# Performance work log

Measured on AMD Instinct MI355X. Metric: run time of the kernel, lower is better.

## Reference

```python
import jax, jax.numpy as jnp
import numpy as np

C0, C1 = 16, 16              # multiplicities of 0e (scalar) and 1o (vector) irreps
FC_DIM = 32
N_EDGE_FEAT = 32
W_NUMEL = C0*C0 + C1*C0 + C0*C1 + C1*C1   # 1024 tensor-product path weights
D_IN = C0 + 3*C1             # 64


def split_irreps(x):
    # layout: [..., C0 scalars | C1 vectors flattened (C1,3)]
    s = x[..., :C0]
    v = x[..., C0:].reshape(x.shape[:-1] + (C1, 3))
    return s, v


def irrep_linear(s, v, ws, wv):
    # e3nn o3.Linear: per-irrep channel mixing, normalized by sqrt(fan_in)
    s2 = jnp.einsum('...i,io->...o', s, ws) / jnp.sqrt(jnp.float32(ws.shape[0]))
    v2 = jnp.einsum('...ix,io->...ox', v, wv) / jnp.sqrt(jnp.float32(wv.shape[0]))
    return s2, v2


def setup_inputs() -> dict:
    key = jax.random.key(0)
    ks = jax.random.split(key, 12)
    B, N = 2, 256
    node_attr = jax.random.normal(ks[0], (B, N, D_IN), jnp.float32)
    edge_attr = jax.random.normal(ks[1], (B, N, N, N_EDGE_FEAT), jnp.float32)
    edge_sh = jax.random.normal(ks[2], (B, N, N, 4), jnp.float32)  # 1x0e + 1x1o
    mask = jnp.ones((B, N), jnp.float32)
    # learned parameters
    w_lin_in_s = jax.random.normal(ks[3], (C0, C0), jnp.float32)
    w_lin_in_v = jax.random.normal(ks[4], (C1, C1), jnp.float32)
    fc_w1 = jax.random.normal(ks[5], (N_EDGE_FEAT, FC_DIM), jnp.float32) / np.sqrt(N_EDGE_FEAT)
    fc_b1 = jnp.zeros((FC_DIM,), jnp.float32)
    fc_w2 = jax.random.normal(ks[6], (FC_DIM, W_NUMEL), jnp.float32) / np.sqrt(FC_DIM)
    fc_b2 = jnp.zeros((W_NUMEL,), jnp.float32)
    w_lin_out_s = jax.random.normal(ks[7], (C0, C0), jnp.float32)
    w_lin_out_v = jax.random.normal(ks[8], (C1, C1), jnp.float32)
    return dict(node_attr=node_attr, edge_attr=edge_attr, edge_sh=edge_sh, mask=mask,
                w_lin_in_s=w_lin_in_s, w_lin_in_v=w_lin_in_v,
                fc_w1=fc_w1, fc_b1=fc_b1, fc_w2=fc_w2, fc_b2=fc_b2,
                w_lin_out_s=w_lin_out_s, w_lin_out_v=w_lin_out_v)


def tp_conv(node_attr, edge_attr, edge_sh, mask, w_lin_in_s, w_lin_in_v,
            fc_w1, fc_b1, fc_w2, fc_b2, w_lin_out_s, w_lin_out_v):
    B, N, _ = node_attr.shape
    s_na, v_na = split_irreps(node_attr)
    # lin_in
    s_in, v_in = irrep_linear(s_na, v_na, w_lin_in_s, w_lin_in_v)  # [B,N,C0], [B,N,C1,3]
    sh_s = edge_sh[..., 0]      # [B,N,N]
    sh_v = edge_sh[..., 1:4]    # [B,N,N,3]
    # edge MLP producing per-edge tensor-product path weights
    h = jax.nn.relu(edge_attr @ fc_w1 + fc_b1)
    w = h @ fc_w2 + fc_b2       # [B,N,N,W_NUMEL]
    off = 0
    w_ss = w[..., off:off+C0*C0].reshape(B, N, N, C0, C0); off += C0*C0
    w_vv = w[..., off:off+C1*C0].reshape(B, N, N, C1, C0); off += C1*C0
    w_sv = w[..., off:off+C0*C1].reshape(B, N, N, C0, C1); off += C0*C1
    w_vs = w[..., off:off+C1*C1].reshape(B, N, N, C1, C1)
    inv_fan = 1.0 / jnp.sqrt(jnp.float32(C0 + C1))
    # --- FullyConnectedTensorProduct (node i features x edge (i,j) SH) ---
    # 0e output: (0e x 0e -> 0e) + (1o x 1o -> 0e, CG = dot/sqrt(3))
    t_ss = jnp.einsum('bni,bnmio->bnmo', s_in, w_ss) * sh_s[..., None]
    dots = jnp.einsum('bnix,bnmx->bnmi', v_in, sh_v)
    t_vv = jnp.einsum('bnmi,bnmio->bnmo', dots, w_vv) / jnp.sqrt(3.0)
    tp_s = (t_ss + t_vv) * inv_fan                                  # [B,N,N,C0]
    # 1o output: (0e x 1o -> 1o) + (1o x 0e -> 1o)
    t_sv = jnp.einsum('bni,bnmio->bnmo', s_in, w_sv)[..., None] * sh_v[:, :, :, None, :]
    t_vs = jnp.einsum('bnix,bnmio->bnmox', v_in, w_vs) * sh_s[..., None, None]
    tp_v = (t_sv + t_vs) * inv_fan                                  # [B,N,N,C1,3]
    # --- masked reduction over source axis j (dim 2), excluding self ---
    m = mask[:, None, :] * (1.0 - jnp.eye(N, dtype=mask.dtype))[None]  # [B,N,N]
    dsum = jnp.sum(mask, axis=-1) - 1.0                                # [B]
    out_s = jnp.einsum('bnmo,bnm->bno', tp_s, m) / dsum[:, None, None]
    out_v = jnp.einsum('bnmox,bnm->bnox', tp_v, m) / dsum[:, None, None, None]
    # lin_out + residual (out dim == in dim, so F.pad is a no-op)
    out_s, out_v = irrep_linear(out_s, out_v, w_lin_out_s, w_lin_out_v)
    out_s = out_s + s_na
    out_v = out_v + v_na
    return jnp.concatenate([out_s, out_v.reshape(out_v.shape[0], out_v.shape[1], C1*3)], axis=-1)


def reference(node_attr, edge_attr, edge_sh, mask, w_lin_in_s, w_lin_in_v,
              fc_w1, fc_b1, fc_w2, fc_b2, w_lin_out_s, w_lin_out_v):
    return tp_conv(node_attr, edge_attr, edge_sh, mask, w_lin_in_s, w_lin_in_v,
                   fc_w1, fc_b1, fc_w2, fc_b2, w_lin_out_s, w_lin_out_v)
```

## Files before the change

kernel.cpp:

```cpp
#include <hip/hip_runtime.h>
#include <hip/hip_bf16.h>

typedef short short8 __attribute__((ext_vector_type(8)));
typedef float f32x4 __attribute__((ext_vector_type(4)));

__device__ __forceinline__ unsigned short f2bf(float f) {
    union { float f; unsigned int i; } v; v.f = f;
    unsigned int i = v.i;
    unsigned int r = (i + 0x7fffu + ((i >> 16) & 1u)) >> 16;
    return (unsigned short)r;
}

__global__ __launch_bounds__(256, 2)
void tpconv_kernel(const float* __restrict__ node_attr,
                   const float* __restrict__ edge_attr,
                   const float* __restrict__ edge_sh,
                   const float* __restrict__ mask,
                   const float* __restrict__ wlis,
                   const float* __restrict__ wliv,
                   const float* __restrict__ fc_w1,
                   const float* __restrict__ fc_b1,
                   const float* __restrict__ fc_w2,
                   const float* __restrict__ fc_b2,
                   const float* __restrict__ wlos,
                   const float* __restrict__ wlov,
                   float* __restrict__ out)
{
    const int node = blockIdx.x;
    const int b = node >> 8;
    const int n = node & 255;
    const int t = threadIdx.x;

    __shared__ __align__(16) unsigned short s_ea[256 * 32];
    __shared__ __align__(16) unsigned short s_w1t[32 * 32];
    __shared__ __align__(16) float s_wc[4 * 256];
    __shared__ float s_b1[32];
    __shared__ float s_wmask[4];
    __shared__ __align__(16) float s_wp[512];
    __shared__ float s_wp0[16];
    __shared__ __align__(16) float s_mom[128];
    __shared__ float s_mom0[4];
    __shared__ float s_scale;
    __shared__ float s_sin[16];
    __shared__ float s_vin[48];
    __shared__ __align__(16) float s_eff[8 * 256];
    __shared__ float s_pre[16];
    __shared__ float s_prev[48];

    {
        const float4* src = (const float4*)(edge_attr + (size_t)node * (256 * 32));
        #pragma unroll
        for (int it = 0; it < 8; ++it) {
            float4 v = src[it * 256 + t];
            ushort4 u;
            u.x = f2bf(v.x); u.y = f2bf(v.y); u.z = f2bf(v.z); u.w = f2bf(v.w);
            *(ushort4*)&s_ea[(it * 256 + t) * 4] = u;
        }
    }
    {
        float mk = mask[(b << 8) + t];
        float ms = mk;
        ms += __shfl_xor(ms, 1);  ms += __shfl_xor(ms, 2);  ms += __shfl_xor(ms, 4);
        ms += __shfl_xor(ms, 8);  ms += __shfl_xor(ms, 16); ms += __shfl_xor(ms, 32);
        if ((t & 63) == 0) s_wmask[t >> 6] = ms;
        float excl = (t == n) ? 0.0f : mk;
        const float4 sh4 = *(const float4*)(edge_sh + ((size_t)node * 256 + t) * 4);
        s_wc[0 * 256 + t] = excl * sh4.x;
        s_wc[1 * 256 + t] = excl * sh4.y;
        s_wc[2 * 256 + t] = excl * sh4.z;
        s_wc[3 * 256 + t] = excl * sh4.w;
    }
    {
        #pragma unroll
        for (int j = 0; j < 4; ++j) {
            int e = t * 4 + j;
            int f = e >> 5, k = e & 31;
            s_w1t[e] = f2bf(fc_w1[k * 32 + f]);
        }
        if (t < 32) s_b1[t] = fc_b1[t];
    }
    if (t >= 64 && t < 80) {
        int o = t - 64;
        const float* na = node_attr + (size_t)node * 64;
        float a = 0.f;
        #pragma unroll
        for (int i = 0; i < 16; ++i) a += na[i] * wlis[i * 16 + o];
        s_sin[o] = a * 0.25f;
    } else if (t >= 80 && t < 128) {
        int idx = t - 80;
        int o = idx / 3, x = idx - o * 3;
        const float* na = node_attr + (size_t)node * 64;
        float a = 0.f;
        #pragma unroll
        for (int i = 0; i < 16; ++i) a += na[16 + i * 3 + x] * wliv[i * 16 + o];
        s_vin[idx] = a * 0.25f;
    }
    __syncthreads();

    {
        const int wv = t >> 6;
        const int ln = t & 63;
        const int q  = ln >> 4;
        const int fc = ln & 15;
        short8 bf0 = *(const short8*)&s_w1t[fc * 32 + q * 8];
        short8 bf1 = *(const short8*)&s_w1t[(16 + fc) * 32 + q * 8];
        float b1a = s_b1[fc], b1b = s_b1[16 + fc];
        float pmc[4][2] = {{0,0},{0,0},{0,0},{0,0}};
        float pm0[4] = {0,0,0,0};
        #pragma unroll
        for (int tt = 0; tt < 4; ++tt) {
            const int T = wv * 4 + tt;
            short8 af = *(const short8*)&s_ea[(T * 16 + fc) * 32 + q * 8];
            f32x4 z = {0.f, 0.f, 0.f, 0.f};
            f32x4 acc0 = __builtin_amdgcn_mfma_f32_16x16x32_bf16(af, bf0, z, 0, 0, 0);
            f32x4 acc1 = __builtin_amdgcn_mfma_f32_16x16x32_bf16(af, bf1, z, 0, 0, 0);
            f32x4 w0 = *(const f32x4*)&s_wc[0 * 256 + T * 16 + q * 4];
            f32x4 w1 = *(const f32x4*)&s_wc[1 * 256 + T * 16 + q * 4];
            f32x4 w2 = *(const f32x4*)&s_wc[2 * 256 + T * 16 + q * 4];
            f32x4 w3 = *(const f32x4*)&s_wc[3 * 256 + T * 16 + q * 4];
            #pragma unroll
            for (int r = 0; r < 4; ++r) {
                float h0 = acc0[r] + b1a; h0 = h0 > 0.f ? h0 : 0.f;
                float h1 = acc1[r] + b1b; h1 = h1 > 0.f ? h1 : 0.f;
                float wr0 = w0[r], wr1 = w1[r], wr2 = w2[r], wr3 = w3[r];
                pmc[0][0] += h0 * wr0; pmc[0][1] += h1 * wr0;
                pmc[1][0] += h0 * wr1; pmc[1][1] += h1 * wr1;
                pmc[2][0] += h0 * wr2; pmc[2][1] += h1 * wr2;
                pmc[3][0] += h0 * wr3; pmc[3][1] += h1 * wr3;
                pm0[0] += wr0; pm0[1] += wr1; pm0[2] += wr2; pm0[3] += wr3;
            }
        }
        #pragma unroll
        for (int c = 0; c < 4; ++c) {
            #pragma unroll
            for (int ft = 0; ft < 2; ++ft) {
                float v = pmc[c][ft];
                v += __shfl_xor(v, 16);
                v += __shfl_xor(v, 32);
                if (q == 0) s_wp[(wv * 4 + c) * 32 + ft * 16 + fc] = v;
            }
            float v0 = pm0[c];
            v0 += __shfl_xor(v0, 16);
            v0 += __shfl_xor(v0, 32);
            if (ln == 0) s_wp0[wv * 4 + c] = v0;
        }
    }
    __syncthreads();

    if (t < 128) {
        int c = t >> 5, f = t & 31;
        s_mom[c * 32 + f] = s_wp[(0 + c) * 32 + f] + s_wp[(4 + c) * 32 + f]
                          + s_wp[(8 + c) * 32 + f] + s_wp[(12 + c) * 32 + f];
    } else if (t == 128) {
        #pragma unroll
        for (int c = 0; c < 4; ++c)
            s_mom0[c] = s_wp0[c] + s_wp0[4 + c] + s_wp0[8 + c] + s_wp0[12 + c];
    } else if (t == 129) {
        float ds = s_wmask[0] + s_wmask[1] + s_wmask[2] + s_wmask[3] - 1.0f;
        s_scale = 0.17677669529663687f / ds;
    }
    __syncthreads();

    {
        const int e8 = t >> 5;
        const int q8 = t & 31;
        const int col0 = q8 * 8;
        int c, wblk;
        if (e8 == 0)      { c = 0;      wblk = 0; }
        else if (e8 <= 3) { c = e8;     wblk = 1; }
        else if (e8 <= 6) { c = e8 - 3; wblk = 2; }
        else              { c = 0;      wblk = 3; }
        float momf[32];
        #pragma unroll
        for (int f = 0; f < 32; ++f) momf[f] = s_mom[c * 32 + f];
        float m0 = s_mom0[c];
        const float* w2g = fc_w2 + wblk * 256 + col0;
        const float* b2g = fc_b2 + wblk * 256 + col0;
        float acc[8];
        float4 bbA = *(const float4*)b2g;
        float4 bbB = *(const float4*)(b2g + 4);
        acc[0] = m0 * bbA.x; acc[1] = m0 * bbA.y; acc[2] = m0 * bbA.z; acc[3] = m0 * bbA.w;
        acc[4] = m0 * bbB.x; acc[5] = m0 * bbB.y; acc[6] = m0 * bbB.z; acc[7] = m0 * bbB.w;
        #pragma unroll
        for (int f = 0; f < 32; ++f) {
            float4 wA = *(const float4*)(w2g + f * 1024);
            float4 wB = *(const float4*)(w2g + f * 1024 + 4);
            float mf = momf[f];
            acc[0] += mf * wA.x; acc[1] += mf * wA.y; acc[2] += mf * wA.z; acc[3] += mf * wA.w;
            acc[4] += mf * wB.x; acc[5] += mf * wB.y; acc[6] += mf * wB.z; acc[7] += mf * wB.w;
        }
        #pragma unroll
        for (int j = 0; j < 8; ++j) s_eff[e8 * 256 + col0 + j] = acc[j];
    }
    __syncthreads();

    {
        const float inv_s3 = 0.5773502691896258f;
        if (t < 16) {
            int o = t;
            float a = 0.f;
            #pragma unroll
            for (int i = 0; i < 16; ++i) a += s_sin[i] * s_eff[0 * 256 + i * 16 + o];
            float bs = 0.f;
            #pragma unroll
            for (int x = 0; x < 3; ++x)
                #pragma unroll
                for (int i = 0; i < 16; ++i)
                    bs += s_vin[i * 3 + x] * s_eff[(1 + x) * 256 + i * 16 + o];
            s_pre[o] = (a + bs * inv_s3) * s_scale;
        } else if (t < 64) {
            int idx = t - 16;
            int o = idx / 3, x = idx - o * 3;
            float a = 0.f;
            #pragma unroll
            for (int i = 0; i < 16; ++i) a += s_sin[i] * s_eff[(4 + x) * 256 + i * 16 + o];
            float bs = 0.f;
            #pragma unroll
            for (int i = 0; i < 16; ++i) bs += s_vin[i * 3 + x] * s_eff[7 * 256 + i * 16 + o];
            s_prev[idx] = (a + bs) * s_scale;
        }
    }
    __syncthreads();

    if (t < 16) {
        int o = t;
        float a = 0.f;
        #pragma unroll
        for (int i = 0; i < 16; ++i) a += s_pre[i] * wlos[i * 16 + o];
        const float* na = node_attr + (size_t)node * 64;
        out[(size_t)node * 64 + o] = a * 0.25f + na[o];
    } else if (t < 64) {
        int idx = t - 16;
        int o = idx / 3, x = idx - o * 3;
        float a = 0.f;
        #pragma unroll
        for (int i = 0; i < 16; ++i) a += s_prev[i * 3 + x] * wlov[i * 16 + o];
        const float* na = node_attr + (size_t)node * 64;
        out[(size_t)node * 64 + 16 + idx] = a * 0.25f + na[16 + idx];
    }
}

extern "C" void kernel_launch(void* const* d_in, const int* in_sizes, int n_in,
                              void* d_out, int out_size, void* d_ws, size_t ws_size,
                              hipStream_t stream) {
    (void)n_in; (void)d_ws; (void)ws_size; (void)out_size;
    const float* node_attr = (const float*)d_in[0];
    const float* edge_attr = (const float*)d_in[1];
    const float* edge_sh   = (const float*)d_in[2];
    const float* maskp     = (const float*)d_in[3];
    const float* wlis      = (const float*)d_in[4];
    const float* wliv      = (const float*)d_in[5];
    const float* fc_w1     = (const float*)d_in[6];
    const float* fc_b1     = (const float*)d_in[7];
    const float* fc_w2     = (const float*)d_in[8];
    const float* fc_b2     = (const float*)d_in[9];
    const float* wlos      = (const float*)d_in[10];
    const float* wlov      = (const float*)d_in[11];
    float* outp = (float*)d_out;

    int nodes = in_sizes[0] / 64;
    tpconv_kernel<<<dim3(nodes), dim3(256), 0, stream>>>(
        node_attr, edge_attr, edge_sh, maskp, wlis, wliv,
        fc_w1, fc_b1, fc_w2, fc_b2, wlos, wlov, outp);
}
```

Baseline: 95.48 us.

## Split fused kernel into per-tile moment kernel and per-node finish kernel

The single per-node kernel is replaced by two launches. The first assigns one wave per 16-edge tile, loads edge features straight from global into MFMA registers without LDS staging, and writes partial moments to workspace. The second reduces those partials and runs the fc_w2 contraction with a rebalanced thread mapping that reuses each weight load across three channels. The intent is more parallelism and less LDS/sync overhead in the bandwidth-bound edge pass, at the cost of an extra launch and a workspace round trip.

```diff
diff --git a/kernel.cpp b/kernel.cpp
--- a/kernel.cpp
+++ b/kernel.cpp
@@ -1,44 +1,110 @@
 #include <hip/hip_runtime.h>
-#include <hip/hip_bf16.h>
 
 typedef short short8 __attribute__((ext_vector_type(8)));
 typedef float f32x4 __attribute__((ext_vector_type(4)));
 
 __device__ __forceinline__ unsigned short f2bf(float f) {
     union { float f; unsigned int i; } v; v.f = f;
-    unsigned int i = v.i;
-    unsigned int r = (i + 0x7fffu + ((i >> 16) & 1u)) >> 16;
-    return (unsigned short)r;
+    return (unsigned short)((v.i + 0x7fffu + ((v.i >> 16) & 1u)) >> 16);
+}
+
+__global__ __launch_bounds__(256, 4)
+void tp_moments(const float* __restrict__ edge_attr,
+                const float* __restrict__ edge_sh,
+                const float* __restrict__ mask,
+                const float* __restrict__ fc_w1,
+                const float* __restrict__ fc_b1,
+                float* __restrict__ part)
+{
+    const int t = threadIdx.x;
+    const int wv = t >> 6, ln = t & 63, q = ln >> 4, fc = ln & 15;
+    const int tile = blockIdx.x * 4 + wv;
+    const int node = tile >> 4;
+    const int T = tile & 15;
+    const int b = node >> 8, n = node & 255;
+    const int e0 = T * 16;
+
+    short8 bf0, bf1;
+    #pragma unroll
+    for (int j = 0; j < 8; ++j) {
+        int k = q * 8 + j;
+        bf0[j] = (short)f2bf(fc_w1[k * 32 + fc]);
+        bf1[j] = (short)f2bf(fc_w1[k * 32 + 16 + fc]);
+    }
+    float b1a = fc_b1[fc], b1b = fc_b1[16 + fc];
+
+    const float* ar = edge_attr + (size_t)node * 8192 + (size_t)(e0 + fc) * 32 + q * 8;
+    float4 a0 = *(const float4*)ar;
+    float4 a1 = *(const float4*)(ar + 4);
+    short8 af;
+    af[0] = (short)f2bf(a0.x); af[1] = (short)f2bf(a0.y);
+    af[2] = (short)f2bf(a0.z); af[3] = (short)f2bf(a0.w);
+    af[4] = (short)f2bf(a1.x); af[5] = (short)f2bf(a1.y);
+    af[6] = (short)f2bf(a1.z); af[7] = (short)f2bf(a1.w);
+
+    float4 mk4 = *(const float4*)(mask + b * 256 + e0 + q * 4);
+    float mkk[4] = { mk4.x, mk4.y, mk4.z, mk4.w };
+    float wc[4][4];
+    #pragma unroll
+    for (int r = 0; r < 4; ++r) {
+        int er = e0 + q * 4 + r;
+        float excl = (er == n) ? 0.f : mkk[r];
+        float4 sh = *(const float4*)(edge_sh + ((size_t)node * 256 + er) * 4);
+        wc[0][r] = excl * sh.x; wc[1][r] = excl * sh.y;
+        wc[2][r] = excl * sh.z; wc[3][r] = excl * sh.w;
+    }
+
+    f32x4 z = { 0.f, 0.f, 0.f, 0.f };
+    f32x4 acc0 = __builtin_amdgcn_mfma_f32_16x16x32_bf16(af, bf0, z, 0, 0, 0);
+    f32x4 acc1 = __builtin_amdgcn_mfma_f32_16x16x32_bf16(af, bf1, z, 0, 0, 0);
+
+    float pmc[4][2] = {{0,0},{0,0},{0,0},{0,0}};
+    float pm0[4] = {0,0,0,0};
+    #pragma unroll
+    for (int r = 0; r < 4; ++r) {
+        float h0 = acc0[r] + b1a; h0 = h0 > 0.f ? h0 : 0.f;
+        float h1 = acc1[r] + b1b; h1 = h1 > 0.f ? h1 : 0.f;
+        #pragma unroll
+        for (int c = 0; c < 4; ++c) {
+            float w = wc[c][r];
+            pmc[c][0] += h0 * w;
+            pmc[c][1] += h1 * w;
+            pm0[c]    += w;
+        }
+    }
+
+    float* pt = part + (size_t)tile * 132;
+    #pragma unroll
+    for (int c = 0; c < 4; ++c) {
+        #pragma unroll
+        for (int ft = 0; ft < 2; ++ft) {
+            float v = pmc[c][ft];
+            v += __shfl_xor(v, 16);
+            v += __shfl_xor(v, 32);
+            if (q == 0) pt[c * 32 + ft * 16 + fc] = v;
+        }
+        float v0 = pm0[c];
+        v0 += __shfl_xor(v0, 16);
+        v0 += __shfl_xor(v0, 32);
+        if (ln == 0) pt[128 + c] = v0;
+    }
 }
 
 __global__ __launch_bounds__(256, 2)
-void tpconv_kernel(const float* __restrict__ node_attr,
-                   const float* __restrict__ edge_attr,
-                   const float* __restrict__ edge_sh,
-                   const float* __restrict__ mask,
-                   const float* __restrict__ wlis,
-                   const float* __restrict__ wliv,
-                   const float* __restrict__ fc_w1,
-                   const float* __restrict__ fc_b1,
-                   const float* __restrict__ fc_w2,
-                   const float* __restrict__ fc_b2,
-                   const float* __restrict__ wlos,
-                   const float* __restrict__ wlov,
-                   float* __restrict__ out)
+void tp_finish(const float* __restrict__ part,
+               const float* __restrict__ node_attr,
+               const float* __restrict__ mask,
+               const float* __restrict__ wlis, const float* __restrict__ wliv,
+               const float* __restrict__ fc_w2,
+               const float* __restrict__ fc_b2,
+               const float* __restrict__ wlos, const float* __restrict__ wlov,
+               float* __restrict__ out)
 {
     const int node = blockIdx.x;
     const int b = node >> 8;
-    const int n = node & 255;
     const int t = threadIdx.x;
 
-    __shared__ __align__(16) unsigned short s_ea[256 * 32];
-    __shared__ __align__(16) unsigned short s_w1t[32 * 32];
-    __shared__ __align__(16) float s_wc[4 * 256];
-    __shared__ float s_b1[32];
-    __shared__ float s_wmask[4];
-    __shared__ __align__(16) float s_wp[512];
-    __shared__ float s_wp0[16];
-    __shared__ __align__(16) float s_mom[128];
+    __shared__ float s_mom[128];
     __shared__ float s_mom0[4];
     __shared__ float s_scale;
     __shared__ float s_sin[16];
@@ -47,150 +113,81 @@
     __shared__ float s_pre[16];
     __shared__ float s_prev[48];
 
-    {
-        const float4* src = (const float4*)(edge_attr + (size_t)node * (256 * 32));
-        #pragma unroll
-        for (int it = 0; it < 8; ++it) {
-            float4 v = src[it * 256 + t];
-            ushort4 u;
-            u.x = f2bf(v.x); u.y = f2bf(v.y); u.z = f2bf(v.z); u.w = f2bf(v.w);
-            *(ushort4*)&s_ea[(it * 256 + t) * 4] = u;
-        }
-    }
-    {
-        float mk = mask[(b << 8) + t];
-        float ms = mk;
+    if (t < 128) {
+        const float* p = part + (size_t)node * 16 * 132 + t;
+        float a = 0.f;
+        #pragma unroll
+        for (int T = 0; T < 16; ++T) a += p[T * 132];
+        s_mom[t] = a;
+    } else if (t < 144) {
+        int o = t - 128;
+        const float* na = node_attr + (size_t)node * 64;
+        float a = 0.f;
+        #pragma unroll
+        for (int i = 0; i < 16; ++i) a += na[i] * wlis[i * 16 + o];
+        s_sin[o] = a * 0.25f;
+    } else if (t < 192) {
+        int idx = t - 144;
+        int o = idx / 3, x = idx - o * 3;
+        const float* na = node_attr + (size_t)node * 64;
+        float a = 0.f;
+        #pragma unroll
+        for (int i = 0; i < 16; ++i) a += na[16 + i * 3 + x] * wliv[i * 16 + o];
+        s_vin[idx] = a * 0.25f;
+    } else {
+        int lane = t - 192;
+        float4 mv = *(const float4*)(mask + b * 256 + lane * 4);
+        float ms = mv.x + mv.y + mv.z + mv.w;
         ms += __shfl_xor(ms, 1);  ms += __shfl_xor(ms, 2);  ms += __shfl_xor(ms, 4);
         ms += __shfl_xor(ms, 8);  ms += __shfl_xor(ms, 16); ms += __shfl_xor(ms, 32);
-        if ((t & 63) == 0) s_wmask[t >> 6] = ms;
-        float excl = (t == n) ? 0.0f : mk;
-        const float4 sh4 = *(const float4*)(edge_sh + ((size_t)node * 256 + t) * 4);
-        s_wc[0 * 256 + t] = excl * sh4.x;
-        s_wc[1 * 256 + t] = excl * sh4.y;
-        s_wc[2 * 256 + t] = excl * sh4.z;
-        s_wc[3 * 256 + t] = excl * sh4.w;
-    }
+        if (lane == 0) s_scale = 0.17677669529663687f / (ms - 1.0f);
+        if (lane >= 16 && lane < 20) {
+            int c = lane - 16;
+            const float* p = part + (size_t)node * 16 * 132 + 128 + c;
+            float a = 0.f;
+            #pragma unroll
+            for (int T = 0; T < 16; ++T) a += p[T * 132];
+            s_mom0[c] = a;
+        }
+    }
+    __syncthreads();
+
     {
-        #pragma unroll
-        for (int j = 0; j < 4; ++j) {
-            int e = t * 4 + j;
-            int f = e >> 5, k = e & 31;
-            s_w1t[e] = f2bf(fc_w1[k * 32 + f]);
-        }
-        if (t < 32) s_b1[t] = fc_b1[t];
-    }
-    if (t >= 64 && t < 80) {
-        int o = t - 64;
-        const float* na = node_attr + (size_t)node * 64;
-        float a = 0.f;
-        #pragma unroll
-        for (int i = 0; i < 16; ++i) a += na[i] * wlis[i * 16 + o];
-        s_sin[o] = a * 0.25f;
-    } else if (t >= 80 && t < 128) {
-        int idx = t - 80;
-        int o = idx / 3, x = idx - o * 3;
-        const float* na = node_attr + (size_t)node * 64;
-        float a = 0.f;
-        #pragma unroll
-        for (int i = 0; i < 16; ++i) a += na[16 + i * 3 + x] * wliv[i * 16 + o];
-        s_vin[idx] = a * 0.25f;
-    }
-    __syncthreads();
-
-    {
-        const int wv = t >> 6;
-        const int ln = t & 63;
-        const int q  = ln >> 4;
-        const int fc = ln & 15;
-        short8 bf0 = *(const short8*)&s_w1t[fc * 32 + q * 8];
-        short8 bf1 = *(const short8*)&s_w1t[(16 + fc) * 32 + q * 8];
-        float b1a = s_b1[fc], b1b = s_b1[16 + fc];
-        float pmc[4][2] = {{0,0},{0,0},{0,0},{0,0}};
-        float pm0[4] = {0,0,0,0};
-        #pragma unroll
-        for (int tt = 0; tt < 4; ++tt) {
-            const int T = wv * 4 + tt;
-            short8 af = *(const short8*)&s_ea[(T * 16 + fc) * 32 + q * 8];
-            f32x4 z = {0.f, 0.f, 0.f, 0.f};
-            f32x4 acc0 = __builtin_amdgcn_mfma_f32_16x16x32_bf16(af, bf0, z, 0, 0, 0);
-            f32x4 acc1 = __builtin_amdgcn_mfma_f32_16x16x32_bf16(af, bf1, z, 0, 0, 0);
-            f32x4 w0 = *(const f32x4*)&s_wc[0 * 256 + T * 16 + q * 4];
-            f32x4 w1 = *(const f32x4*)&s_wc[1 * 256 + T * 16 + q * 4];
-            f32x4 w2 = *(const f32x4*)&s_wc[2 * 256 + T * 16 + q * 4];
-            f32x4 w3 = *(const f32x4*)&s_wc[3 * 256 + T * 16 + q * 4];
-            #pragma unroll
-            for (int r = 0; r < 4; ++r) {
-                float h0 = acc0[r] + b1a; h0 = h0 > 0.f ? h0 : 0.f;
-                float h1 = acc1[r] + b1b; h1 = h1 > 0.f ? h1 : 0.f;
-                float wr0 = w0[r], wr1 = w1[r], wr2 = w2[r], wr3 = w3[r];
-                pmc[0][0] += h0 * wr0; pmc[0][1] += h1 * wr0;
-                pmc[1][0] += h0 * wr1; pmc[1][1] += h1 * wr1;
-                pmc[2][0] += h0 * wr2; pmc[2][1] += h1 * wr2;
-                pmc[3][0] += h0 * wr3; pmc[3][1] += h1 * wr3;
-                pm0[0] += wr0; pm0[1] += wr1; pm0[2] += wr2; pm0[3] += wr3;
+        const int wblk = t >> 6;
+        const int col0 = (t & 63) * 4;
+        const float* w2g = fc_w2 + wblk * 256 + col0;
+        float4 bb = *(const float4*)(fc_b2 + wblk * 256 + col0);
+        if (wblk == 0 || wblk == 3) {
+            float m0 = s_mom0[0];
+            float a0 = m0 * bb.x, a1 = m0 * bb.y, a2 = m0 * bb.z, a3 = m0 * bb.w;
+            #pragma unroll 4
+            for (int f = 0; f < 32; ++f) {
+                float4 w = *(const float4*)(w2g + f * 1024);
+                float mf = s_mom[f];
+                a0 += mf * w.x; a1 += mf * w.y; a2 += mf * w.z; a3 += mf * w.w;
             }
-        }
-        #pragma unroll
-        for (int c = 0; c < 4; ++c) {
-            #pragma unroll
-            for (int ft = 0; ft < 2; ++ft) {
-                float v = pmc[c][ft];
-                v += __shfl_xor(v, 16);
-                v += __shfl_xor(v, 32);
-                if (q == 0) s_wp[(wv * 4 + c) * 32 + ft * 16 + fc] = v;
+            float* d = s_eff + ((wblk == 0) ? 0 : 7) * 256 + col0;
+            d[0] = a0; d[1] = a1; d[2] = a2; d[3] = a3;
+        } else {
+            float m1 = s_mom0[1], m2 = s_mom0[2], m3 = s_mom0[3];
+            float A1[4] = { m1*bb.x, m1*bb.y, m1*bb.z, m1*bb.w };
+            float A2[4] = { m2*bb.x, m2*bb.y, m2*bb.z, m2*bb.w };
+            float A3[4] = { m3*bb.x, m3*bb.y, m3*bb.z, m3*bb.w };
+            #pragma unroll 4
+            for (int f = 0; f < 32; ++f) {
+                float4 w = *(const float4*)(w2g + f * 1024);
+                float mf1 = s_mom[32 + f], mf2 = s_mom[64 + f], mf3 = s_mom[96 + f];
+                A1[0] += mf1 * w.x; A1[1] += mf1 * w.y; A1[2] += mf1 * w.z; A1[3] += mf1 * w.w;
+                A2[0] += mf2 * w.x; A2[1] += mf2 * w.y; A2[2] += mf2 * w.z; A2[3] += mf2 * w.w;
+                A3[0] += mf3 * w.x; A3[1] += mf3 * w.y; A3[2] += mf3 * w.z; A3[3] += mf3 * w.w;
             }
-            float v0 = pm0[c];
-            v0 += __shfl_xor(v0, 16);
-            v0 += __shfl_xor(v0, 32);
-            if (ln == 0) s_wp0[wv * 4 + c] = v0;
-        }
-    }
-    __syncthreads();
-
-    if (t < 128) {
-        int c = t >> 5, f = t & 31;
-        s_mom[c * 32 + f] = s_wp[(0 + c) * 32 + f] + s_wp[(4 + c) * 32 + f]
-                          + s_wp[(8 + c) * 32 + f] + s_wp[(12 + c) * 32 + f];
-    } else if (t == 128) {
-        #pragma unroll
-        for (int c = 0; c < 4; ++c)
-            s_mom0[c] = s_wp0[c] + s_wp0[4 + c] + s_wp0[8 + c] + s_wp0[12 + c];
-    } else if (t == 129) {
-        float ds = s_wmask[0] + s_wmask[1] + s_wmask[2] + s_wmask[3] - 1.0f;
-        s_scale = 0.17677669529663687f / ds;
-    }
-    __syncthreads();
-
-    {
-        const int e8 = t >> 5;
-        const int q8 = t & 31;
-        const int col0 = q8 * 8;
-        int c, wblk;
-        if (e8 == 0)      { c = 0;      wblk = 0; }
-        else if (e8 <= 3) { c = e8;     wblk = 1; }
-        else if (e8 <= 6) { c = e8 - 3; wblk = 2; }
-        else              { c = 0;      wblk = 3; }
-        float momf[32];
-        #pragma unroll
-        for (int f = 0; f < 32; ++f) momf[f] = s_mom[c * 32 + f];
-        float m0 = s_mom0[c];
-        const float* w2g = fc_w2 + wblk * 256 + col0;
-        const float* b2g = fc_b2 + wblk * 256 + col0;
-        float acc[8];
-        float4 bbA = *(const float4*)b2g;
-        float4 bbB = *(const float4*)(b2g + 4);
-        acc[0] = m0 * bbA.x; acc[1] = m0 * bbA.y; acc[2] = m0 * bbA.z; acc[3] = m0 * bbA.w;
-        acc[4] = m0 * bbB.x; acc[5] = m0 * bbB.y; acc[6] = m0 * bbB.z; acc[7] = m0 * bbB.w;
-        #pragma unroll
-        for (int f = 0; f < 32; ++f) {
-            float4 wA = *(const float4*)(w2g + f * 1024);
-            float4 wB = *(const float4*)(w2g + f * 1024 + 4);
-            float mf = momf[f];
-            acc[0] += mf * wA.x; acc[1] += mf * wA.y; acc[2] += mf * wA.z; acc[3] += mf * wA.w;
-            acc[4] += mf * wB.x; acc[5] += mf * wB.y; acc[6] += mf * wB.z; acc[7] += mf * wB.w;
-        }
-        #pragma unroll
-        for (int j = 0; j < 8; ++j) s_eff[e8 * 256 + col0 + j] = acc[j];
+            int e8b = (wblk == 1) ? 1 : 4;
+            float* d1 = s_eff + (e8b + 0) * 256 + col0;
+            float* d2 = s_eff + (e8b + 1) * 256 + col0;
+            float* d3 = s_eff + (e8b + 2) * 256 + col0;
+            #pragma unroll
+            for (int j = 0; j < 4; ++j) { d1[j] = A1[j]; d2[j] = A2[j]; d3[j] = A3[j]; }
+        }
     }
     __syncthreads();
 
@@ -243,7 +240,7 @@
 extern "C" void kernel_launch(void* const* d_in, const int* in_sizes, int n_in,
                               void* d_out, int out_size, void* d_ws, size_t ws_size,
                               hipStream_t stream) {
-    (void)n_in; (void)d_ws; (void)ws_size; (void)out_size;
+    (void)n_in; (void)ws_size; (void)out_size;
     const float* node_attr = (const float*)d_in[0];
     const float* edge_attr = (const float*)d_in[1];
     const float* edge_sh   = (const float*)d_in[2];
@@ -257,9 +254,11 @@
     const float* wlos      = (const float*)d_in[10];
     const float* wlov      = (const float*)d_in[11];
     float* outp = (float*)d_out;
+    float* part = (float*)d_ws;
 
     int nodes = in_sizes[0] / 64;
-    tpconv_kernel<<<dim3(nodes), dim3(256), 0, stream>>>(
-        node_attr, edge_attr, edge_sh, maskp, wlis, wliv,
-        fc_w1, fc_b1, fc_w2, fc_b2, wlos, wlov, outp);
-}
+    tp_moments<<<dim3(nodes * 4), dim3(256), 0, stream>>>(
+        edge_attr, edge_sh, maskp, fc_w1, fc_b1, part);
+    tp_finish<<<dim3(nodes), dim3(256), 0, stream>>>(
+        part, node_attr, maskp, wlis, wliv, fc_w2, fc_b2, wlos, wlov, outp);
+}
```

After: 96.98 us. About the same (+1.6%).
